# Optimization experiments

Measured on AMD Instinct MI355X. Metric: run time of the kernel, lower is better.

## Reference

```python
import jax, jax.numpy as jnp
import numpy as np

K_MAX = 16
SCALE = 1.0 / (32 * 32)


def setup_inputs() -> dict:
    key = jax.random.key(0)
    k1, k2, k3 = jax.random.split(key, 3)
    B, C_in, C_out, H, W = 16, 32, 32, 256, 256
    x = jax.random.normal(k1, (B, C_in, H, W), dtype=jnp.float32)
    weights_real = SCALE * jax.random.normal(k2, (C_in, C_out, K_MAX, K_MAX), dtype=jnp.float32)
    weights_imag = SCALE * jax.random.normal(k3, (C_in, C_out, K_MAX, K_MAX), dtype=jnp.float32)
    return {"x": x, "weights_real": weights_real, "weights_imag": weights_imag}


def reference(x, weights_real, weights_imag):
    B, C, H, W = x.shape
    C_out = weights_real.shape[1]
    k = min(K_MAX, H, W // 2 + 1)
    x_ft = jnp.fft.rfft2(x, norm='ortho')                 # (B, C, H, W//2+1) complex64
    w = (weights_real + 1j * weights_imag)[:, :, :k, :k]  # (C, C_out, k, k)
    # Faithful to original einsum 'bijk,ijkm->bkm' with broadcast over the
    # size-1 i/j slices: sums x_ft over its ROW axis; x_ft's COLUMN index
    # becomes the output-block row index.
    S = jnp.sum(x_ft[:, :, :k, :k], axis=2)               # (B, C, k)  indexed by freq column
    blk = jnp.einsum('bir,iorc->borc', S, w)              # (B, C_out, k, k)
    out_ft = jnp.zeros((B, C_out, H, W // 2 + 1), dtype=x_ft.dtype)
    out_ft = out_ft.at[:, :, :k, :k].set(blk)
    return jnp.fft.irfft2(out_ft, s=(H, W), norm='ortho')
```

## Files before the change

kernel.cpp:

```cpp
#include <hip/hip_runtime.h>
#include <math.h>


#define TWO_PI_OVER_256 0.02454369260617026

typedef __attribute__((ext_vector_type(8))) short short8;
typedef __attribute__((ext_vector_type(4))) float f32x4;

static __device__ inline void bf16split(unsigned short* h, unsigned short* l, float a)
{
    const unsigned u = __builtin_bit_cast(unsigned, a);
    const unsigned short hs = (unsigned short)(u >> 16);
    *h = hs;
    const float fh = __builtin_bit_cast(float, (unsigned)hs << 16);
    const float lo = a - fh;
    *l = (unsigned short)(__builtin_bit_cast(unsigned, lo) >> 16);
}

__global__ __launch_bounds__(256) void k0_tables(float* __restrict__ tbl,
                                                 unsigned short* __restrict__ tswz)
{
    const int t = threadIdx.x;
    const int blk = blockIdx.x;
    if (blk == 0) {
        const double a = TWO_PI_OVER_256 * (double)t;
        tbl[t]       = (float)cos(a);
        tbl[256 + t] = (float)sin(a);
        return;
    }
    const int ct = blk - 1;
    for (int e = t; e < 1024; e += 256) {
        const int term = e >> 9;
        const int lane = (e >> 3) & 63;
        const int j = e & 7;
        const int k = ((lane >> 4) << 3) + j;
        const int x = (ct << 4) + (lane & 15);
        const int v = (k < 16) ? k : (k - 16);
        const double ang = TWO_PI_OVER_256 * (double)((v * x) & 255);
        const float val = (float)((k < 16) ? cos(ang) : sin(ang));
        const unsigned ubits = __builtin_bit_cast(unsigned, val);
        const unsigned short hi = (unsigned short)(ubits >> 16);
        unsigned short wbits;
        if (term == 0) {
            wbits = hi;
        } else {
            const float fhi = __builtin_bit_cast(float, (unsigned)hi << 16);
            const float lo = val - fhi;
            wbits = (unsigned short)(__builtin_bit_cast(unsigned, lo) >> 16);
        }
        tswz[((term * 16 + ct) * 64 + lane) * 8 + j] = wbits;
    }
}

__global__ __launch_bounds__(256) void k1_partial(
    const float* __restrict__ x, const float* __restrict__ tbl,
    float* __restrict__ s_part)
{
    __shared__ float twc[256], tws[256];
    __shared__ float gre[64], gim[64];
    __shared__ float Pre[4][256], Pim[4][256];
    __shared__ float red_re[16][16], red_im[16][16];

    const int t = threadIdx.x;
    const int blk = blockIdx.x;
    const int bi = blk >> 2, chunk = blk & 3;
    const int y0 = chunk << 6;

    twc[t] = tbl[t];
    tws[t] = tbl[256 + t];
    __syncthreads();
    if (t < 64) {
        const int h = y0 + t;
        float gr = 0.f, gi = 0.f;
        #pragma unroll
        for (int u = 0; u < 16; ++u) {
            const int idx = (u * h) & 255;
            gr += twc[idx];
            gi -= tws[idx];
        }
        gre[t] = gr; gim[t] = gi;
    }
    __syncthreads();

    const float* img = x + (size_t)bi * 65536 + (size_t)y0 * 256;
    const int cg = t & 63, rg = t >> 6;
    float4 pr = {0.f,0.f,0.f,0.f}, pi = {0.f,0.f,0.f,0.f};
    #pragma unroll 4
    for (int k = 0; k < 16; ++k) {
        const int hl = rg + (k << 2);
        const float4 xv = *(const float4*)(img + (hl << 8) + (cg << 2));
        const float gr = gre[hl], gi = gim[hl];
        pr.x += gr * xv.x; pr.y += gr * xv.y; pr.z += gr * xv.z; pr.w += gr * xv.w;
        pi.x += gi * xv.x; pi.y += gi * xv.y; pi.z += gi * xv.z; pi.w += gi * xv.w;
    }
    *(float4*)&Pre[rg][cg << 2] = pr;
    *(float4*)&Pim[rg][cg << 2] = pi;
    __syncthreads();

    {
        const float sr = Pre[0][t] + Pre[1][t] + Pre[2][t] + Pre[3][t];
        const float si = Pim[0][t] + Pim[1][t] + Pim[2][t] + Pim[3][t];
        Pre[0][t] = sr;
        Pim[0][t] = si;
    }
    __syncthreads();

    {
        const int v = t >> 4, j = t & 15;
        const int i0 = (v * j) & 255;
        float c = twc[i0], s = tws[i0];
        const int id = (v << 4) & 255;
        const float cd = twc[id], sd = tws[id];
        float ar = 0.f, ai = 0.f;
        #pragma unroll
        for (int m = 0; m < 16; ++m) {
            const int w = j + (m << 4);
            const float prr = Pre[0][w];
            const float pii = Pim[0][w];
            ar += prr * c + pii * s;
            ai += pii * c - prr * s;
            const float nc = c * cd - s * sd;
            const float ns = s * cd + c * sd;
            c = nc; s = ns;
        }
        red_re[v][j] = ar; red_im[v][j] = ai;
    }
    __syncthreads();
    if (t < 16) {
        const float4* rr4 = (const float4*)&red_re[t][0];
        const float4* ri4 = (const float4*)&red_im[t][0];
        float ar = 0.f, ai = 0.f;
        #pragma unroll
        for (int q = 0; q < 4; ++q) {
            const float4 a = rr4[q], b = ri4[q];
            ar += a.x + a.y + a.z + a.w;
            ai += b.x + b.y + b.z + b.w;
        }
        float* sp = s_part + (size_t)bi * 128 + chunk * 32;
        sp[t]      = ar * (1.0f / 256.0f);
        sp[t + 16] = ai * (1.0f / 256.0f);
    }
}

__global__ __launch_bounds__(256) void k23_synth(
    const float* __restrict__ wr, const float* __restrict__ wi,
    const float* __restrict__ s_part, const float* __restrict__ tbl,
    const unsigned short* __restrict__ tswz,
    float* __restrict__ out)
{
    __shared__ float twc[256], tws[256];
    __shared__ float Sre[32][16], Sim[32][16];
    __shared__ float Btr[16 * 20], Bti[16 * 20];
    __shared__ __align__(16) unsigned short Ah[64 * 40], Al[64 * 40];

    const int t = threadIdx.x;
    const int blk = blockIdx.x;
    const int bo = blk >> 2;
    const int y0 = (blk & 3) << 6;
    const int b = bo >> 5, o = bo & 31;

    twc[t] = tbl[t];
    tws[t] = tbl[256 + t];
    {
        const float* sb = s_part + (size_t)b * 4096;
        #pragma unroll
        for (int e = t; e < 512; e += 256) {
            const int i = e >> 4, u = e & 15;
            const float* p = sb + i * 128 + u;
            Sre[i][u] = p[0] + p[32] + p[64] + p[96];
            Sim[i][u] = p[16] + p[48] + p[80] + p[112];
        }
    }
    __syncthreads();

    {
        const int u = t >> 4, v = t & 15;
        float br = 0.f, bim = 0.f;
        const float* wrp = wr + o * 256 + t;
        const float* wip = wi + o * 256 + t;
        #pragma unroll 8
        for (int i = 0; i < 32; ++i) {
            const float a_re = Sre[i][u], a_im = Sim[i][u];
            const float w_re = wrp[i * 8192], w_im = wip[i * 8192];
            br  += a_re * w_re - a_im * w_im;
            bim += a_re * w_im + a_im * w_re;
        }
        Btr[v * 20 + u] = br;
        Bti[v * 20 + u] = bim;
    }
    __syncthreads();

    {
        const int v = t & 15, slot = t >> 4;
        float br[16], bim[16];
        const float4* bpr = (const float4*)&Btr[v * 20];
        const float4* bpi = (const float4*)&Bti[v * 20];
        #pragma unroll
        for (int q = 0; q < 4; ++q) {
            const float4 r4 = bpr[q], i4 = bpi[q];
            br[q*4+0]  = r4.x; br[q*4+1]  = r4.y; br[q*4+2]  = r4.z; br[q*4+3]  = r4.w;
            bim[q*4+0] = i4.x; bim[q*4+1] = i4.y; bim[q*4+2] = i4.z; bim[q*4+3] = i4.w;
        }
        const float scale = (v == 0) ? (1.0f / 256.0f) : (1.0f / 128.0f);
        #pragma unroll
        for (int m = 0; m < 4; ++m) {
            const int r = slot * 4 + m;
            const int y = y0 + r;
            const float c1 = twc[y], s1 = tws[y];
            float gr = br[0], gi = bim[0];
            float cc = 1.f, cs = 0.f;
            #pragma unroll
            for (int u = 1; u < 16; ++u) {
                const float nc = cc * c1 - cs * s1;
                const float ns = cc * s1 + cs * c1;
                cc = nc; cs = ns;
                gr += br[u] * cc - bim[u] * cs;
                gi += br[u] * cs + bim[u] * cc;
            }
            const float a0 = gr * scale;
            const float a1 = (v == 0) ? 0.f : (-gi * scale);
            bf16split(&Ah[r * 40 + v],      &Al[r * 40 + v],      a0);
            bf16split(&Ah[r * 40 + 16 + v], &Al[r * 40 + 16 + v], a1);
        }
    }
    __syncthreads();

    {
        const int lane = t & 63, wv = t >> 6;
        short8 afh[4], afl[4];
        #pragma unroll
        for (int m = 0; m < 4; ++m) {
            const int off = (m * 16 + (lane & 15)) * 40 + ((lane >> 4) << 3);
            afh[m] = *(const short8*)&Ah[off];
            afl[m] = *(const short8*)&Al[off];
        }
        float* outb = out + (size_t)bo * 65536 + (size_t)y0 * 256;
        #pragma unroll
        for (int q = 0; q < 4; ++q) {
            const int ct = (wv << 2) + q;
            const short8 bh = *(const short8*)&tswz[(size_t)(ct * 64 + lane) * 8];
            const short8 bl = *(const short8*)&tswz[(size_t)((16 + ct) * 64 + lane) * 8];
            #pragma unroll
            for (int m = 0; m < 4; ++m) {
                f32x4 acc = {0.f, 0.f, 0.f, 0.f};
                acc = __builtin_amdgcn_mfma_f32_16x16x32_bf16(afh[m], bh, acc, 0, 0, 0);
                acc = __builtin_amdgcn_mfma_f32_16x16x32_bf16(afh[m], bl, acc, 0, 0, 0);
                acc = __builtin_amdgcn_mfma_f32_16x16x32_bf16(afl[m], bh, acc, 0, 0, 0);
                float* op = outb + (size_t)(16 * m + ((lane >> 4) << 2)) * 256
                                 + (ct << 4) + (lane & 15);
                #pragma unroll
                for (int reg = 0; reg < 4; ++reg)
                    __builtin_nontemporal_store(acc[reg], op + reg * 256);
            }
        }
    }
}

extern "C" void kernel_launch(void* const* d_in, const int* in_sizes, int n_in,
                              void* d_out, int out_size, void* d_ws, size_t ws_size,
                              hipStream_t stream) {
    (void)in_sizes; (void)n_in; (void)out_size; (void)ws_size;
    const float* x  = (const float*)d_in[0];
    const float* wr = (const float*)d_in[1];
    const float* wi = (const float*)d_in[2];
    float* out    = (float*)d_out;
    float* s_part = (float*)d_ws;
    float* tbl    = s_part + 65536;
    unsigned short* tswz = (unsigned short*)(tbl + 512);

    k0_tables<<<17, 256, 0, stream>>>(tbl, tswz);
    k1_partial<<<2048, 256, 0, stream>>>(x, tbl, s_part);
    k23_synth<<<2048, 256, 0, stream>>>(wr, wi, s_part, tbl, tswz, out);
}
```

Baseline: 255.9 us.

## Move row-axis inverse DFT to bf16 MFMA with precomputed twiddle tables

```diff
diff --git a/kernel.cpp b/kernel.cpp
--- a/kernel.cpp
+++ b/kernel.cpp
@@ -17,44 +17,65 @@
     *l = (unsigned short)(__builtin_bit_cast(unsigned, lo) >> 16);
 }
 
-__global__ __launch_bounds__(256) void k0_tables(float* __restrict__ tbl,
-                                                 unsigned short* __restrict__ tswz)
-{
+__global__ __launch_bounds__(256) void k0_tables(
+    float* __restrict__ tbl, float* __restrict__ gtab,
+    unsigned short* __restrict__ tswz, unsigned short* __restrict__ eswz)
+{
+    __shared__ float ctb[256], stb[256];
     const int t = threadIdx.x;
     const int blk = blockIdx.x;
+    {
+        const double a = TWO_PI_OVER_256 * (double)t;
+        ctb[t] = (float)cos(a);
+        stb[t] = (float)sin(a);
+    }
+    __syncthreads();
     if (blk == 0) {
-        const double a = TWO_PI_OVER_256 * (double)t;
-        tbl[t]       = (float)cos(a);
-        tbl[256 + t] = (float)sin(a);
-        return;
-    }
-    const int ct = blk - 1;
-    for (int e = t; e < 1024; e += 256) {
-        const int term = e >> 9;
-        const int lane = (e >> 3) & 63;
-        const int j = e & 7;
-        const int k = ((lane >> 4) << 3) + j;
-        const int x = (ct << 4) + (lane & 15);
-        const int v = (k < 16) ? k : (k - 16);
-        const double ang = TWO_PI_OVER_256 * (double)((v * x) & 255);
-        const float val = (float)((k < 16) ? cos(ang) : sin(ang));
-        const unsigned ubits = __builtin_bit_cast(unsigned, val);
-        const unsigned short hi = (unsigned short)(ubits >> 16);
-        unsigned short wbits;
-        if (term == 0) {
-            wbits = hi;
-        } else {
-            const float fhi = __builtin_bit_cast(float, (unsigned)hi << 16);
-            const float lo = val - fhi;
-            wbits = (unsigned short)(__builtin_bit_cast(unsigned, lo) >> 16);
-        }
-        tswz[((term * 16 + ct) * 64 + lane) * 8 + j] = wbits;
+        tbl[t]       = ctb[t];
+        tbl[256 + t] = stb[t];
+        float gr = 0.f, gi = 0.f;
+        #pragma unroll
+        for (int u = 0; u < 16; ++u) {
+            const int idx = (u * t) & 255;
+            gr += ctb[idx];
+            gi -= stb[idx];
+        }
+        gtab[2 * t]     = gr;
+        gtab[2 * t + 1] = gi;
+    } else if (blk <= 16) {
+        const int ct = blk - 1;
+        for (int e = t; e < 1024; e += 256) {
+            const int term = e >> 9, lane = (e >> 3) & 63, j = e & 7;
+            const int k = ((lane >> 4) << 3) + j;
+            const int x = (ct << 4) + (lane & 15);
+            const int v = (k < 16) ? k : (k - 16);
+            const int idx = (v * x) & 255;
+            const float val = (k < 16) ? ctb[idx] : stb[idx];
+            unsigned short hb, lb; bf16split(&hb, &lb, val);
+            tswz[((term * 16 + ct) * 64 + lane) * 8 + j] = term ? lb : hb;
+        }
+    } else {
+        for (int e = t; e < 1024; e += 256) {
+            const int gid = (blk - 17) * 1024 + e;
+            const int j = gid & 7, lane = (gid >> 3) & 63;
+            const int yt = (gid >> 9) & 15, pt = gid >> 13;
+            const int p = pt >> 1, term = pt & 1;
+            const int y = (yt << 4) + (lane & 15);
+            const int k = ((lane >> 4) << 3) + j;
+            const int v = (k < 16) ? k : (k - 16);
+            const int idx = (v * y) & 255;
+            float val;
+            if (p == 0) val = (k < 16) ? ctb[idx] : -stb[idx];
+            else        val = (k < 16) ? stb[idx] :  ctb[idx];
+            unsigned short hb, lb; bf16split(&hb, &lb, val);
+            eswz[gid] = term ? lb : hb;
+        }
     }
 }
 
 __global__ __launch_bounds__(256) void k1_partial(
     const float* __restrict__ x, const float* __restrict__ tbl,
-    float* __restrict__ s_part)
+    const float* __restrict__ gtab, float* __restrict__ s_part)
 {
     __shared__ float twc[256], tws[256];
     __shared__ float gre[64], gim[64];
@@ -68,17 +89,9 @@
 
     twc[t] = tbl[t];
     tws[t] = tbl[256 + t];
-    __syncthreads();
     if (t < 64) {
-        const int h = y0 + t;
-        float gr = 0.f, gi = 0.f;
-        #pragma unroll
-        for (int u = 0; u < 16; ++u) {
-            const int idx = (u * h) & 255;
-            gr += twc[idx];
-            gi -= tws[idx];
-        }
-        gre[t] = gr; gim[t] = gi;
+        const float2 g = *(const float2*)(gtab + ((y0 + t) << 1));
+        gre[t] = g.x; gim[t] = g.y;
     }
     __syncthreads();
 
@@ -144,23 +157,20 @@
 
 __global__ __launch_bounds__(256) void k23_synth(
     const float* __restrict__ wr, const float* __restrict__ wi,
-    const float* __restrict__ s_part, const float* __restrict__ tbl,
+    const float* __restrict__ s_part,
     const unsigned short* __restrict__ tswz,
+    const unsigned short* __restrict__ eswz,
     float* __restrict__ out)
 {
-    __shared__ float twc[256], tws[256];
     __shared__ float Sre[32][16], Sim[32][16];
-    __shared__ float Btr[16 * 20], Bti[16 * 20];
+    __shared__ __align__(16) unsigned short Bfh[512], Bfl[512];
     __shared__ __align__(16) unsigned short Ah[64 * 40], Al[64 * 40];
 
     const int t = threadIdx.x;
     const int blk = blockIdx.x;
     const int bo = blk >> 2;
-    const int y0 = (blk & 3) << 6;
     const int b = bo >> 5, o = bo & 31;
 
-    twc[t] = tbl[t];
-    tws[t] = tbl[256 + t];
     {
         const float* sb = s_part + (size_t)b * 4096;
         #pragma unroll
@@ -185,42 +195,42 @@
             br  += a_re * w_re - a_im * w_im;
             bim += a_re * w_im + a_im * w_re;
         }
-        Btr[v * 20 + u] = br;
-        Bti[v * 20 + u] = bim;
-    }
-    __syncthreads();
-
-    {
-        const int v = t & 15, slot = t >> 4;
-        float br[16], bim[16];
-        const float4* bpr = (const float4*)&Btr[v * 20];
-        const float4* bpi = (const float4*)&Bti[v * 20];
-        #pragma unroll
-        for (int q = 0; q < 4; ++q) {
-            const float4 r4 = bpr[q], i4 = bpi[q];
-            br[q*4+0]  = r4.x; br[q*4+1]  = r4.y; br[q*4+2]  = r4.z; br[q*4+3]  = r4.w;
-            bim[q*4+0] = i4.x; bim[q*4+1] = i4.y; bim[q*4+2] = i4.z; bim[q*4+3] = i4.w;
-        }
+        unsigned short h0, l0, h1, l1;
+        bf16split(&h0, &l0, br);
+        bf16split(&h1, &l1, bim);
+        const int lr = ((((u >> 3) << 4) | v) << 3) + (u & 7);
+        const int li = ((((2 + (u >> 3)) << 4) | v) << 3) + (u & 7);
+        Bfh[lr] = h0; Bfl[lr] = l0;
+        Bfh[li] = h1; Bfl[li] = l1;
+    }
+    __syncthreads();
+
+    {
+        const int lane = t & 63, wv = t >> 6;
+        const int yt = ((blk & 3) << 2) + wv;
+        const short8 bh = *(const short8*)&Bfh[lane << 3];
+        const short8 bl = *(const short8*)&Bfl[lane << 3];
+        const short8 arh = *(const short8*)&eswz[(size_t)(( 0 + yt) << 9) + (lane << 3)];
+        const short8 arl = *(const short8*)&eswz[(size_t)((16 + yt) << 9) + (lane << 3)];
+        const short8 aih = *(const short8*)&eswz[(size_t)((32 + yt) << 9) + (lane << 3)];
+        const short8 ail = *(const short8*)&eswz[(size_t)((48 + yt) << 9) + (lane << 3)];
+        f32x4 gre = {0.f, 0.f, 0.f, 0.f}, gim = {0.f, 0.f, 0.f, 0.f};
+        gre = __builtin_amdgcn_mfma_f32_16x16x32_bf16(arh, bh, gre, 0, 0, 0);
+        gre = __builtin_amdgcn_mfma_f32_16x16x32_bf16(arh, bl, gre, 0, 0, 0);
+        gre = __builtin_amdgcn_mfma_f32_16x16x32_bf16(arl, bh, gre, 0, 0, 0);
+        gim = __builtin_amdgcn_mfma_f32_16x16x32_bf16(aih, bh, gim, 0, 0, 0);
+        gim = __builtin_amdgcn_mfma_f32_16x16x32_bf16(aih, bl, gim, 0, 0, 0);
+        gim = __builtin_amdgcn_mfma_f32_16x16x32_bf16(ail, bh, gim, 0, 0, 0);
+        const int v = lane & 15;
         const float scale = (v == 0) ? (1.0f / 256.0f) : (1.0f / 128.0f);
-        #pragma unroll
-        for (int m = 0; m < 4; ++m) {
-            const int r = slot * 4 + m;
-            const int y = y0 + r;
-            const float c1 = twc[y], s1 = tws[y];
-            float gr = br[0], gi = bim[0];
-            float cc = 1.f, cs = 0.f;
-            #pragma unroll
-            for (int u = 1; u < 16; ++u) {
-                const float nc = cc * c1 - cs * s1;
-                const float ns = cc * s1 + cs * c1;
-                cc = nc; cs = ns;
-                gr += br[u] * cc - bim[u] * cs;
-                gi += br[u] * cs + bim[u] * cc;
-            }
-            const float a0 = gr * scale;
-            const float a1 = (v == 0) ? 0.f : (-gi * scale);
-            bf16split(&Ah[r * 40 + v],      &Al[r * 40 + v],      a0);
-            bf16split(&Ah[r * 40 + 16 + v], &Al[r * 40 + 16 + v], a1);
+        const int rbase = (wv << 4) + ((lane >> 4) << 2);
+        #pragma unroll
+        for (int reg = 0; reg < 4; ++reg) {
+            const int r = rbase + reg;
+            const float cc = gre[reg] * scale;
+            const float cs = (v == 0) ? 0.f : (-gim[reg] * scale);
+            bf16split(&Ah[r * 40 + v],      &Al[r * 40 + v],      cc);
+            bf16split(&Ah[r * 40 + 16 + v], &Al[r * 40 + 16 + v], cs);
         }
     }
     __syncthreads();
@@ -234,7 +244,7 @@
             afh[m] = *(const short8*)&Ah[off];
             afl[m] = *(const short8*)&Al[off];
         }
-        float* outb = out + (size_t)bo * 65536 + (size_t)y0 * 256;
+        float* outb = out + (size_t)bo * 65536 + (size_t)((blk & 3) << 6) * 256;
         #pragma unroll
         for (int q = 0; q < 4; ++q) {
             const int ct = (wv << 2) + q;
@@ -266,9 +276,11 @@
     float* out    = (float*)d_out;
     float* s_part = (float*)d_ws;
     float* tbl    = s_part + 65536;
-    unsigned short* tswz = (unsigned short*)(tbl + 512);
-
-    k0_tables<<<17, 256, 0, stream>>>(tbl, tswz);
-    k1_partial<<<2048, 256, 0, stream>>>(x, tbl, s_part);
-    k23_synth<<<2048, 256, 0, stream>>>(wr, wi, s_part, tbl, tswz, out);
-}
+    float* gtab   = tbl + 512;
+    unsigned short* tswz = (unsigned short*)(gtab + 512);
+    unsigned short* eswz = tswz + 16384;
+
+    k0_tables<<<49, 256, 0, stream>>>(tbl, gtab, tswz, eswz);
+    k1_partial<<<2048, 256, 0, stream>>>(x, tbl, gtab, s_part);
+    k23_synth<<<2048, 256, 0, stream>>>(wr, wi, s_part, tswz, eswz, out);
+}
```

After: 252.4 us. About the same (-1.4%).
